# Kernel tuning notes

Hardware: AMD Instinct MI355X
Metric: run time of the kernel (lower is better)

## Reference

```python
import jax, jax.numpy as jnp
import numpy as np

HEADS = 8
DIM_HEAD = 64
SCALE = DIM_HEAD ** -0.5


def setup_inputs() -> dict:
    key = jax.random.key(0)
    ks = jax.random.split(key, 6)
    B, S, D = 4, 2048, 512
    return {
        "hidden_states": jax.random.normal(ks[0], (B, S, D), jnp.float32),
        "Wq": jax.random.normal(ks[1], (D, D), jnp.float32) * (D ** -0.5),
        "Wk": jax.random.normal(ks[2], (D, D), jnp.float32) * (D ** -0.5),
        "Wv": jax.random.normal(ks[3], (D, D), jnp.float32) * (D ** -0.5),
        "Wo": jax.random.normal(ks[4], (D, D), jnp.float32) * (D ** -0.5),
        "bo": jnp.zeros((D,), jnp.float32),
    }


def reference(hidden_states, Wq, Wk, Wv, Wo, bo):
    B, S, D = hidden_states.shape
    H, Dh = HEADS, DIM_HEAD
    # Linear projections (torch Linear: x @ W.T; weights here stored as [D, D] used directly)
    q = hidden_states @ Wq  # [B,S,D]
    k = hidden_states @ Wk
    v = hidden_states @ Wv
    # head_to_batch_dim: [B,S,D] -> [B,H,S,Dh]
    q = q.reshape(B, S, H, Dh).transpose(0, 2, 1, 3)
    k = k.reshape(B, S, H, Dh).transpose(0, 2, 1, 3)
    v = v.reshape(B, S, H, Dh).transpose(0, 2, 1, 3)
    # scaled dot-product attention, scores materialized as in baddbmm path
    scores = jnp.einsum("bhqd,bhkd->bhqk", q, k) * SCALE  # [B,H,S,S]
    probs = jax.nn.softmax(scores, axis=-1)
    out = jnp.einsum("bhqk,bhkd->bhqd", probs, v)  # [B,H,S,Dh]
    # batch_to_head_dim: [B,H,S,Dh] -> [B,S,D]
    out = out.transpose(0, 2, 1, 3).reshape(B, S, D)
    # output projection (Dropout with p=0 is identity)
    return out @ Wo + bo
```

## Files before the change

kernel.cpp:

```cpp
#include <hip/hip_runtime.h>
#include <cstdint>
#include <cstddef>


typedef __bf16 bf16;
typedef __bf16 bf16x4_t __attribute__((ext_vector_type(4)));
typedef __bf16 bf16x8_t __attribute__((ext_vector_type(8)));
typedef float  floatx4  __attribute__((ext_vector_type(4)));
typedef short  shortx4  __attribute__((ext_vector_type(4)));

#define NB   4
#define SEQ  2048
#define DM   512
#define NH   8
#define DH   64
#define MTOT (NB * SEQ)


__device__ __forceinline__ void gload16(const void* g, void* l) {
    __builtin_amdgcn_global_load_lds((const __attribute__((address_space(1))) unsigned int*)g,
                                     (__attribute__((address_space(3))) unsigned int*)l,
                                     16, 0, 0);
}

__device__ __forceinline__ shortx4 pack4(floatx4 v) {
    union { bf16x4_t h; shortx4 s; } u;
    u.h = (bf16x4_t){ (bf16)v[0], (bf16)v[1], (bf16)v[2], (bf16)v[3] };
    return u.s;
}

__global__ __launch_bounds__(256) void cvt_x(const float* __restrict__ x, bf16* __restrict__ xb) {
    int i = (blockIdx.x * 256 + threadIdx.x) * 4;
    float4 v = *(const float4*)(x + i);
    bf16x4_t o = { (bf16)v.x, (bf16)v.y, (bf16)v.z, (bf16)v.w };
    *(bf16x4_t*)(xb + i) = o;
}

__global__ __launch_bounds__(256) void prep_w(const float* __restrict__ Wq, const float* __restrict__ Wk,
                                              const float* __restrict__ Wv, const float* __restrict__ Wo,
                                              bf16* __restrict__ Wqkvt, bf16* __restrict__ Wot) {
    __shared__ float T[64][65];
    const int tid = threadIdx.x;
    const int m = blockIdx.z;
    const int k0 = blockIdx.x * 64, n0 = blockIdx.y * 64;
    const float* W = (m == 0) ? Wq : (m == 1) ? Wk : (m == 2) ? Wv : Wo;
    const float scale = (m == 0) ? 0.18033688011112042f : 1.0f;
#pragma unroll
    for (int p = 0; p < 4; p++) {
        int row = p * 16 + (tid >> 4), col = (tid & 15) * 4;
        float4 v = *(const float4*)(W + (size_t)(k0 + row) * DM + n0 + col);
        T[row][col + 0] = v.x * scale; T[row][col + 1] = v.y * scale;
        T[row][col + 2] = v.z * scale; T[row][col + 3] = v.w * scale;
    }
    __syncthreads();
#pragma unroll
    for (int p = 0; p < 4; p++) {
        int nr = p * 16 + (tid >> 4), kc = (tid & 15) * 4;
        bf16x4_t o = { (bf16)T[kc][nr], (bf16)T[kc + 1][nr], (bf16)T[kc + 2][nr], (bf16)T[kc + 3][nr] };
        bf16* dst = (m < 3) ? (Wqkvt + ((size_t)(m * DM + n0 + nr)) * DM + k0 + kc)
                            : (Wot + (size_t)(n0 + nr) * DM + k0 + kc);
        *(bf16x4_t*)dst = o;
    }
}

__global__ __launch_bounds__(256) void gemm_bt(
        const bf16* __restrict__ A, const bf16* __restrict__ Bt, int Kd, int mode,
        bf16* __restrict__ Qh, bf16* __restrict__ Kh, bf16* __restrict__ Vt,
        const float* __restrict__ bo, float* __restrict__ out) {
    __shared__ __attribute__((aligned(16))) bf16 As[128 * 64];
    __shared__ __attribute__((aligned(16))) bf16 Bs[128 * 64];
    const int tid = threadIdx.x;
    const int wave = tid >> 6, lane = tid & 63;
    const int l15 = lane & 15, quad = lane >> 4, h7 = l15 & 7;
    const int m0 = blockIdx.x * 128, n0 = blockIdx.y * 128;
    const int mw = (wave >> 1) * 64, nw = (wave & 1) * 64;
    const int srow = lane >> 3, sc = (lane & 7) ^ srow;

    floatx4 zero = {0.f, 0.f, 0.f, 0.f};
    floatx4 acc[4][4];
#pragma unroll
    for (int i = 0; i < 4; i++)
#pragma unroll
        for (int j = 0; j < 4; j++) acc[i][j] = zero;

    for (int k0 = 0; k0 < Kd; k0 += 64) {
#pragma unroll
        for (int t = 0; t < 4; t++) {
            int row = wave * 32 + t * 8 + srow;
            gload16(A  + (size_t)(m0 + row) * Kd + k0 + sc * 8, As + (wave * 32 + t * 8) * 64);
            gload16(Bt + (size_t)(n0 + row) * Kd + k0 + sc * 8, Bs + (wave * 32 + t * 8) * 64);
        }
        __syncthreads();
#pragma unroll
        for (int ks = 0; ks < 2; ks++) {
            bf16x8_t af[4], bfr[4];
#pragma unroll
            for (int i = 0; i < 4; i++)
                af[i] = *(const bf16x8_t*)(As + (mw + i * 16 + l15) * 64 + (((ks * 4 + quad) ^ h7) * 8));
#pragma unroll
            for (int j = 0; j < 4; j++)
                bfr[j] = *(const bf16x8_t*)(Bs + (nw + j * 16 + l15) * 64 + (((ks * 4 + quad) ^ h7) * 8));
#pragma unroll
            for (int i = 0; i < 4; i++)
#pragma unroll
                for (int j = 0; j < 4; j++)
                    acc[i][j] = __builtin_amdgcn_mfma_f32_16x16x32_bf16(af[i], bfr[j], acc[i][j], 0, 0, 0);
        }
        __syncthreads();
    }

#pragma unroll
    for (int i = 0; i < 4; i++) {
#pragma unroll
        for (int j = 0; j < 4; j++) {
#pragma unroll
            for (int r = 0; r < 4; r++) {
                int m = m0 + mw + i * 16 + quad * 4 + r;
                int n = n0 + nw + j * 16 + l15;
                float v = acc[i][j][r];
                if (mode == 0) {
                    int b = m >> 11, s = m & (SEQ - 1);
                    int sect = n >> 9, h = (n >> 6) & 7, d = n & 63;
                    size_t bhh = (size_t)(b * NH + h);
                    if (sect == 0)      Qh[(bhh * SEQ + s) * DH + d] = (bf16)v;
                    else if (sect == 1) Kh[(bhh * SEQ + s) * DH + d] = (bf16)v;
                    else                Vt[(bhh * DH + d) * SEQ + s] = (bf16)v;
                } else {
                    out[(size_t)m * DM + n] = v + bo[n];
                }
            }
        }
    }
}

__global__ __launch_bounds__(256) void flash_attn(
        const bf16* __restrict__ Q, const bf16* __restrict__ Kh,
        const bf16* __restrict__ Vt, bf16* __restrict__ Ob) {
    __shared__ __attribute__((aligned(16))) bf16 KV[2][2][64 * 64];
    const int tid = threadIdx.x;
    const int wave = tid >> 6, lane = tid & 63;
    const int l15 = lane & 15, quad = lane >> 4, h7 = l15 & 7;
    const int qt = blockIdx.x & 15, bh = blockIdx.x >> 4;
    const int q0 = qt * 128;
    const bf16* Kb = Kh + (size_t)bh * SEQ * DH;
    const bf16* Vb = Vt + (size_t)bh * DH * SEQ;

    bf16x8_t aq[2][2];
#pragma unroll
    for (int sub = 0; sub < 2; sub++) {
        const bf16* qr = Q + ((size_t)bh * SEQ + q0 + wave * 32 + sub * 16 + l15) * DH;
        aq[sub][0] = *(const bf16x8_t*)(qr + quad * 8);
        aq[sub][1] = *(const bf16x8_t*)(qr + 32 + quad * 8);
    }

    const int srow = lane >> 3, sc = (lane & 7) ^ srow;
    auto stage = [&](int buf, int kv0) {
#pragma unroll
        for (int t = 0; t < 2; t++) {
            int row = wave * 16 + t * 8 + srow;
            gload16(Kb + (size_t)(kv0 + row) * DH + sc * 8, &KV[buf][0][(wave * 16 + t * 8) * 64]);
            gload16(Vb + (size_t)row * SEQ + kv0 + sc * 8,  &KV[buf][1][(wave * 16 + t * 8) * 64]);
        }
    };

    floatx4 zero = {0.f, 0.f, 0.f, 0.f};
    floatx4 oacc[2][4];
    float l_run[2] = {0.f, 0.f};
#pragma unroll
    for (int sub = 0; sub < 2; sub++)
#pragma unroll
        for (int d = 0; d < 4; d++) oacc[sub][d] = zero;

    stage(0, 0);
    for (int it = 0; it < SEQ / 64; it++) {
        __syncthreads();
        if (it + 1 < SEQ / 64) stage((it + 1) & 1, (it + 1) * 64);
        const bf16* Ks = &KV[it & 1][0][0];
        const bf16* Vs = &KV[it & 1][1][0];

        floatx4 st[2][4];
#pragma unroll
        for (int ns = 0; ns < 4; ns++) {
            const bf16* kr = Ks + (ns * 16 + l15) * 64;
            bf16x8_t k0 = *(const bf16x8_t*)(kr + ((quad ^ h7) * 8));
            bf16x8_t k1 = *(const bf16x8_t*)(kr + (((4 + quad) ^ h7) * 8));
#pragma unroll
            for (int sub = 0; sub < 2; sub++) {
                floatx4 a = zero;
                a = __builtin_amdgcn_mfma_f32_16x16x32_bf16(k0, aq[sub][0], a, 0, 0, 0);
                a = __builtin_amdgcn_mfma_f32_16x16x32_bf16(k1, aq[sub][1], a, 0, 0, 0);
                st[sub][ns] = a;
            }
        }
#pragma unroll
        for (int sub = 0; sub < 2; sub++) {
            float s = 0.f;
#pragma unroll
            for (int ns = 0; ns < 4; ns++) {
#pragma unroll
                for (int r = 0; r < 4; r++) {
                    float p = __builtin_amdgcn_exp2f(st[sub][ns][r]);
                    st[sub][ns][r] = p;
                    s += p;
                }
            }
            l_run[sub] += s;
        }
#pragma unroll
        for (int c = 0; c < 4; c++) {
            shortx4 ap[2];
#pragma unroll
            for (int sub = 0; sub < 2; sub++) ap[sub] = pack4(st[sub][c]);
#pragma unroll
            for (int d = 0; d < 4; d++) {
                const bf16* vr = Vs + (d * 16 + l15) * 64;
                int cc = 2 * c + (quad >> 1);
                shortx4 bv = *(const shortx4*)(vr + ((cc ^ h7) * 8) + (quad & 1) * 4);
#pragma unroll
                for (int sub = 0; sub < 2; sub++)
                    oacc[sub][d] = __builtin_amdgcn_mfma_f32_16x16x16bf16_1k(ap[sub], bv, oacc[sub][d], 0, 0, 0);
            }
        }
    }

    float lf[2];
#pragma unroll
    for (int sub = 0; sub < 2; sub++) {
        float l = l_run[sub];
        l += __shfl_xor(l, 16, 64);
        l += __shfl_xor(l, 32, 64);
        lf[sub] = l;
    }
    const int b = bh >> 3, h = bh & 7;
#pragma unroll
    for (int sub = 0; sub < 2; sub++) {
        float linv[4];
#pragma unroll
        for (int r = 0; r < 4; r++) linv[r] = 1.0f / __shfl(lf[sub], quad * 4 + r, 64);
#pragma unroll
        for (int d = 0; d < 4; d++)
#pragma unroll
            for (int r = 0; r < 4; r++) {
                int s = q0 + wave * 32 + sub * 16 + quad * 4 + r;
                Ob[((size_t)b * SEQ + s) * DM + h * DH + d * 16 + l15] = (bf16)(oacc[sub][d][r] * linv[r]);
            }
    }
}

extern "C" void kernel_launch(void* const* d_in, const int* in_sizes, int n_in,
                              void* d_out, int out_size, void* d_ws, size_t ws_size,
                              hipStream_t stream) {
    const float* X  = (const float*)d_in[0];
    const float* Wq = (const float*)d_in[1];
    const float* Wk = (const float*)d_in[2];
    const float* Wv = (const float*)d_in[3];
    const float* Wo = (const float*)d_in[4];
    const float* bo = (const float*)d_in[5];
    float* out = (float*)d_out;

    char* ws = (char*)d_ws;
    bf16* Xb    = (bf16*)(ws + 0);
    bf16* Wqkvt = (bf16*)(ws + 8388608);
    bf16* Wot   = (bf16*)(ws + 9961472);
    bf16* Qh    = (bf16*)(ws + 10485760);
    bf16* Kh    = (bf16*)(ws + 18874368);
    bf16* Vt    = (bf16*)(ws + 27262976);
    bf16* Ob    = (bf16*)(ws + 35651584);

    cvt_x<<<MTOT * DM / 1024, 256, 0, stream>>>(X, Xb);
    prep_w<<<dim3(8, 8, 4), 256, 0, stream>>>(Wq, Wk, Wv, Wo, Wqkvt, Wot);
    gemm_bt<<<dim3(MTOT / 128, 1536 / 128), 256, 0, stream>>>(Xb, Wqkvt, DM, 0,
                                                              Qh, Kh, Vt, nullptr, nullptr);
    flash_attn<<<NB * NH * (SEQ / 128), 256, 0, stream>>>(Qh, Kh, Vt, Ob);
    gemm_bt<<<dim3(MTOT / 128, DM / 128), 256, 0, stream>>>(Ob, Wot, DM, 1,
                                                            nullptr, nullptr, nullptr, bo, out);
}
```

Measured before the change: 185.2 us.

## Split KV across wave pairs in attention and coalesce GEMM epilogues via LDS

Flash attention now gives each wave 64 query rows and half of every KV tile. It stages two KV tiles per barrier and merges the partial accumulators and row sums through shared memory at the end. The QKV projection stages its output tile in LDS so Q/K/V (including transposed V) are written with 16-byte coalesced stores instead of scattered 2-byte writes. The output projection uses smaller 64-row tiles to launch more blocks. This adds register pressure and a final LDS reduction step in attention.

```diff
diff --git a/kernel.cpp b/kernel.cpp
--- a/kernel.cpp
+++ b/kernel.cpp
@@ -8,6 +8,7 @@
 typedef __bf16 bf16x8_t __attribute__((ext_vector_type(8)));
 typedef float  floatx4  __attribute__((ext_vector_type(4)));
 typedef short  shortx4  __attribute__((ext_vector_type(4)));
+typedef uint32_t u32x4  __attribute__((ext_vector_type(4)));
 
 #define NB   4
 #define SEQ  2048
@@ -63,12 +64,11 @@
     }
 }
 
-__global__ __launch_bounds__(256) void gemm_bt(
-        const bf16* __restrict__ A, const bf16* __restrict__ Bt, int Kd, int mode,
-        bf16* __restrict__ Qh, bf16* __restrict__ Kh, bf16* __restrict__ Vt,
-        const float* __restrict__ bo, float* __restrict__ out) {
-    __shared__ __attribute__((aligned(16))) bf16 As[128 * 64];
-    __shared__ __attribute__((aligned(16))) bf16 Bs[128 * 64];
+__global__ __launch_bounds__(256) void gemm_qkv(
+        const bf16* __restrict__ A, const bf16* __restrict__ Bt,
+        bf16* __restrict__ Qh, bf16* __restrict__ Kh, bf16* __restrict__ Vt) {
+    __shared__ __attribute__((aligned(16))) bf16 Sm[2][128 * 64];
+    bf16* As = Sm[0]; bf16* Bs = Sm[1];
     const int tid = threadIdx.x;
     const int wave = tid >> 6, lane = tid & 63;
     const int l15 = lane & 15, quad = lane >> 4, h7 = l15 & 7;
@@ -83,12 +83,12 @@
 #pragma unroll
         for (int j = 0; j < 4; j++) acc[i][j] = zero;
 
-    for (int k0 = 0; k0 < Kd; k0 += 64) {
+    for (int k0 = 0; k0 < DM; k0 += 64) {
 #pragma unroll
         for (int t = 0; t < 4; t++) {
             int row = wave * 32 + t * 8 + srow;
-            gload16(A  + (size_t)(m0 + row) * Kd + k0 + sc * 8, As + (wave * 32 + t * 8) * 64);
-            gload16(Bt + (size_t)(n0 + row) * Kd + k0 + sc * 8, Bs + (wave * 32 + t * 8) * 64);
+            gload16(A  + (size_t)(m0 + row) * DM + k0 + sc * 8, As + (wave * 32 + t * 8) * 64);
+            gload16(Bt + (size_t)(n0 + row) * DM + k0 + sc * 8, Bs + (wave * 32 + t * 8) * 64);
         }
         __syncthreads();
 #pragma unroll
@@ -109,46 +109,140 @@
         __syncthreads();
     }
 
-#pragma unroll
-    for (int i = 0; i < 4; i++) {
-#pragma unroll
-        for (int j = 0; j < 4; j++) {
-#pragma unroll
-            for (int r = 0; r < 4; r++) {
-                int m = m0 + mw + i * 16 + quad * 4 + r;
-                int n = n0 + nw + j * 16 + l15;
-                float v = acc[i][j][r];
-                if (mode == 0) {
-                    int b = m >> 11, s = m & (SEQ - 1);
-                    int sect = n >> 9, h = (n >> 6) & 7, d = n & 63;
-                    size_t bhh = (size_t)(b * NH + h);
-                    if (sect == 0)      Qh[(bhh * SEQ + s) * DH + d] = (bf16)v;
-                    else if (sect == 1) Kh[(bhh * SEQ + s) * DH + d] = (bf16)v;
-                    else                Vt[(bhh * DH + d) * SEQ + s] = (bf16)v;
-                } else {
-                    out[(size_t)m * DM + n] = v + bo[n];
-                }
-            }
-        }
-    }
-}
-
-__global__ __launch_bounds__(256) void flash_attn(
-        const bf16* __restrict__ Q, const bf16* __restrict__ Kh,
-        const bf16* __restrict__ Vt, bf16* __restrict__ Ob) {
-    __shared__ __attribute__((aligned(16))) bf16 KV[2][2][64 * 64];
+    bf16* E = (bf16*)Sm;
+    const int sect = n0 >> 9;
+    const int bq = m0 >> 11;
+    if (sect < 3 && (n0 >> 9) != 2) {}
+    if (sect != 2) {
+        bf16* dstbase = (sect == 0) ? Qh : Kh;
+#pragma unroll
+        for (int p = 0; p < 2; p++) {
+            if ((wave >> 1) == p) {
+#pragma unroll
+                for (int i = 0; i < 4; i++)
+#pragma unroll
+                    for (int j = 0; j < 4; j++)
+#pragma unroll
+                        for (int r = 0; r < 4; r++)
+                            E[(i * 16 + quad * 4 + r) * 136 + nw + j * 16 + l15] = (bf16)acc[i][j][r];
+            }
+            __syncthreads();
+#pragma unroll
+            for (int pp = 0; pp < 4; pp++) {
+                int idx = pp * 256 + tid;
+                int rowl = idx >> 4, chunk = idx & 15;
+                u32x4 v = *(const u32x4*)(E + rowl * 136 + chunk * 8);
+                int mm = m0 + p * 64 + rowl;
+                int s = mm & (SEQ - 1);
+                int n = n0 + chunk * 8;
+                int h = (n >> 6) & 7, d = n & 63;
+                *(u32x4*)(dstbase + (((size_t)(bq * NH + h)) * SEQ + s) * DH + d) = v;
+            }
+            __syncthreads();
+        }
+    } else {
+#pragma unroll
+        for (int p = 0; p < 2; p++) {
+            if ((wave & 1) == p) {
+#pragma unroll
+                for (int i = 0; i < 4; i++)
+#pragma unroll
+                    for (int j = 0; j < 4; j++)
+                        *(shortx4*)(E + (j * 16 + l15) * 136 + mw + i * 16 + quad * 4) = pack4(acc[i][j]);
+            }
+            __syncthreads();
+#pragma unroll
+            for (int pp = 0; pp < 4; pp++) {
+                int idx = pp * 256 + tid;
+                int rowl = idx >> 4, chunk = idx & 15;
+                u32x4 v = *(const u32x4*)(E + rowl * 136 + chunk * 8);
+                int n = n0 + p * 64 + rowl;
+                int h = (n >> 6) & 7, d = n & 63;
+                int s = (m0 & (SEQ - 1)) + chunk * 8;
+                *(u32x4*)(Vt + (((size_t)(bq * NH + h)) * DH + d) * SEQ + s) = v;
+            }
+            __syncthreads();
+        }
+    }
+}
+
+__global__ __launch_bounds__(256) void gemm_out(
+        const bf16* __restrict__ A, const bf16* __restrict__ Bt,
+        const float* __restrict__ bo, float* __restrict__ out) {
+    __shared__ __attribute__((aligned(16))) bf16 As[64 * 64];
+    __shared__ __attribute__((aligned(16))) bf16 Bs[128 * 64];
     const int tid = threadIdx.x;
     const int wave = tid >> 6, lane = tid & 63;
     const int l15 = lane & 15, quad = lane >> 4, h7 = l15 & 7;
+    const int m0 = blockIdx.x * 64, n0 = blockIdx.y * 128;
+    const int nw = wave * 32;
+    const int srow = lane >> 3, sc = (lane & 7) ^ srow;
+
+    floatx4 zero = {0.f, 0.f, 0.f, 0.f};
+    floatx4 acc[4][2];
+#pragma unroll
+    for (int i = 0; i < 4; i++)
+#pragma unroll
+        for (int j = 0; j < 2; j++) acc[i][j] = zero;
+
+    for (int k0 = 0; k0 < DM; k0 += 64) {
+#pragma unroll
+        for (int t = 0; t < 2; t++) {
+            int row = wave * 16 + t * 8 + srow;
+            gload16(A + (size_t)(m0 + row) * DM + k0 + sc * 8, As + (wave * 16 + t * 8) * 64);
+        }
+#pragma unroll
+        for (int t = 0; t < 4; t++) {
+            int row = wave * 32 + t * 8 + srow;
+            gload16(Bt + (size_t)(n0 + row) * DM + k0 + sc * 8, Bs + (wave * 32 + t * 8) * 64);
+        }
+        __syncthreads();
+#pragma unroll
+        for (int ks = 0; ks < 2; ks++) {
+            bf16x8_t af[4], bfr[2];
+#pragma unroll
+            for (int i = 0; i < 4; i++)
+                af[i] = *(const bf16x8_t*)(As + (i * 16 + l15) * 64 + (((ks * 4 + quad) ^ h7) * 8));
+#pragma unroll
+            for (int j = 0; j < 2; j++)
+                bfr[j] = *(const bf16x8_t*)(Bs + (nw + j * 16 + l15) * 64 + (((ks * 4 + quad) ^ h7) * 8));
+#pragma unroll
+            for (int i = 0; i < 4; i++)
+#pragma unroll
+                for (int j = 0; j < 2; j++)
+                    acc[i][j] = __builtin_amdgcn_mfma_f32_16x16x32_bf16(af[i], bfr[j], acc[i][j], 0, 0, 0);
+        }
+        __syncthreads();
+    }
+#pragma unroll
+    for (int i = 0; i < 4; i++)
+#pragma unroll
+        for (int j = 0; j < 2; j++)
+#pragma unroll
+            for (int r = 0; r < 4; r++) {
+                int m = m0 + i * 16 + quad * 4 + r;
+                int n = n0 + nw + j * 16 + l15;
+                out[(size_t)m * DM + n] = acc[i][j][r] + bo[n];
+            }
+}
+
+__global__ __launch_bounds__(256, 2) void flash_attn(
+        const bf16* __restrict__ Q, const bf16* __restrict__ Kh,
+        const bf16* __restrict__ Vt, bf16* __restrict__ Ob) {
+    __shared__ __attribute__((aligned(16))) bf16 SMEM[4 * 8192];
+    const int tid = threadIdx.x;
+    const int wave = tid >> 6, lane = tid & 63;
+    const int l15 = lane & 15, quad = lane >> 4, h7 = l15 & 7;
+    const int qh = wave >> 1, kvh = wave & 1;
     const int qt = blockIdx.x & 15, bh = blockIdx.x >> 4;
     const int q0 = qt * 128;
     const bf16* Kb = Kh + (size_t)bh * SEQ * DH;
     const bf16* Vb = Vt + (size_t)bh * DH * SEQ;
 
-    bf16x8_t aq[2][2];
-#pragma unroll
-    for (int sub = 0; sub < 2; sub++) {
-        const bf16* qr = Q + ((size_t)bh * SEQ + q0 + wave * 32 + sub * 16 + l15) * DH;
+    bf16x8_t aq[4][2];
+#pragma unroll
+    for (int sub = 0; sub < 4; sub++) {
+        const bf16* qr = Q + ((size_t)bh * SEQ + q0 + qh * 64 + sub * 16 + l15) * DH;
         aq[sub][0] = *(const bf16x8_t*)(qr + quad * 8);
         aq[sub][1] = *(const bf16x8_t*)(qr + 32 + quad * 8);
     }
@@ -157,93 +251,128 @@
     auto stage = [&](int buf, int kv0) {
 #pragma unroll
         for (int t = 0; t < 2; t++) {
-            int row = wave * 16 + t * 8 + srow;
-            gload16(Kb + (size_t)(kv0 + row) * DH + sc * 8, &KV[buf][0][(wave * 16 + t * 8) * 64]);
-            gload16(Vb + (size_t)row * SEQ + kv0 + sc * 8,  &KV[buf][1][(wave * 16 + t * 8) * 64]);
+            int rb = wave * 16 + t * 8;
+            gload16(Kb + (size_t)(kv0 + rb + srow) * DH + sc * 8, SMEM + buf * 8192 + rb * 64);
+            gload16(Vb + (size_t)(rb + srow) * SEQ + kv0 + sc * 8, SMEM + buf * 8192 + 4096 + rb * 64);
         }
     };
 
     floatx4 zero = {0.f, 0.f, 0.f, 0.f};
-    floatx4 oacc[2][4];
-    float l_run[2] = {0.f, 0.f};
-#pragma unroll
-    for (int sub = 0; sub < 2; sub++)
+    floatx4 oacc[4][4];
+    float l_run[4] = {0.f, 0.f, 0.f, 0.f};
+#pragma unroll
+    for (int sub = 0; sub < 4; sub++)
 #pragma unroll
         for (int d = 0; d < 4; d++) oacc[sub][d] = zero;
 
     stage(0, 0);
-    for (int it = 0; it < SEQ / 64; it++) {
+    stage(1, 64);
+    for (int seg = 0; seg < 16; seg++) {
         __syncthreads();
-        if (it + 1 < SEQ / 64) stage((it + 1) & 1, (it + 1) * 64);
-        const bf16* Ks = &KV[it & 1][0][0];
-        const bf16* Vs = &KV[it & 1][1][0];
-
-        floatx4 st[2][4];
-#pragma unroll
-        for (int ns = 0; ns < 4; ns++) {
-            const bf16* kr = Ks + (ns * 16 + l15) * 64;
-            bf16x8_t k0 = *(const bf16x8_t*)(kr + ((quad ^ h7) * 8));
-            bf16x8_t k1 = *(const bf16x8_t*)(kr + (((4 + quad) ^ h7) * 8));
-#pragma unroll
-            for (int sub = 0; sub < 2; sub++) {
-                floatx4 a = zero;
-                a = __builtin_amdgcn_mfma_f32_16x16x32_bf16(k0, aq[sub][0], a, 0, 0, 0);
-                a = __builtin_amdgcn_mfma_f32_16x16x32_bf16(k1, aq[sub][1], a, 0, 0, 0);
-                st[sub][ns] = a;
-            }
-        }
-#pragma unroll
-        for (int sub = 0; sub < 2; sub++) {
-            float s = 0.f;
-#pragma unroll
-            for (int ns = 0; ns < 4; ns++) {
-#pragma unroll
-                for (int r = 0; r < 4; r++) {
-                    float p = __builtin_amdgcn_exp2f(st[sub][ns][r]);
-                    st[sub][ns][r] = p;
-                    s += p;
+        if (seg < 15) {
+            stage((2 * seg + 2) & 3, (2 * seg + 2) * 64);
+            stage((2 * seg + 3) & 3, (2 * seg + 3) * 64);
+        }
+#pragma unroll
+        for (int half = 0; half < 2; half++) {
+            const bf16* Ks = SMEM + ((2 * seg + half) & 3) * 8192;
+            const bf16* Vs = Ks + 4096;
+            floatx4 st[4][2];
+#pragma unroll
+            for (int nsl = 0; nsl < 2; nsl++) {
+                int row = (kvh * 2 + nsl) * 16 + l15;
+                const bf16* kr = Ks + row * 64;
+                bf16x8_t k0 = *(const bf16x8_t*)(kr + ((quad ^ h7) * 8));
+                bf16x8_t k1 = *(const bf16x8_t*)(kr + (((4 + quad) ^ h7) * 8));
+#pragma unroll
+                for (int sub = 0; sub < 4; sub++) {
+                    floatx4 a = zero;
+                    a = __builtin_amdgcn_mfma_f32_16x16x32_bf16(k0, aq[sub][0], a, 0, 0, 0);
+                    a = __builtin_amdgcn_mfma_f32_16x16x32_bf16(k1, aq[sub][1], a, 0, 0, 0);
+                    st[sub][nsl] = a;
                 }
             }
-            l_run[sub] += s;
-        }
-#pragma unroll
-        for (int c = 0; c < 4; c++) {
-            shortx4 ap[2];
-#pragma unroll
-            for (int sub = 0; sub < 2; sub++) ap[sub] = pack4(st[sub][c]);
-#pragma unroll
-            for (int d = 0; d < 4; d++) {
-                const bf16* vr = Vs + (d * 16 + l15) * 64;
+#pragma unroll
+            for (int sub = 0; sub < 4; sub++) {
+                float s = 0.f;
+#pragma unroll
+                for (int nsl = 0; nsl < 2; nsl++)
+#pragma unroll
+                    for (int r = 0; r < 4; r++) {
+                        float p = __builtin_amdgcn_exp2f(st[sub][nsl][r]);
+                        st[sub][nsl][r] = p;
+                        s += p;
+                    }
+                l_run[sub] += s;
+            }
+#pragma unroll
+            for (int cl = 0; cl < 2; cl++) {
+                int c = kvh * 2 + cl;
+                shortx4 ap[4];
+#pragma unroll
+                for (int sub = 0; sub < 4; sub++) ap[sub] = pack4(st[sub][cl]);
                 int cc = 2 * c + (quad >> 1);
-                shortx4 bv = *(const shortx4*)(vr + ((cc ^ h7) * 8) + (quad & 1) * 4);
-#pragma unroll
-                for (int sub = 0; sub < 2; sub++)
-                    oacc[sub][d] = __builtin_amdgcn_mfma_f32_16x16x16bf16_1k(ap[sub], bv, oacc[sub][d], 0, 0, 0);
-            }
-        }
-    }
-
-    float lf[2];
-#pragma unroll
-    for (int sub = 0; sub < 2; sub++) {
+#pragma unroll
+                for (int d = 0; d < 4; d++) {
+                    const bf16* vr = Vs + (d * 16 + l15) * 64;
+                    shortx4 bv = *(const shortx4*)(vr + ((cc ^ h7) * 8) + (quad & 1) * 4);
+#pragma unroll
+                    for (int sub = 0; sub < 4; sub++)
+                        oacc[sub][d] = __builtin_amdgcn_mfma_f32_16x16x16bf16_1k(ap[sub], bv, oacc[sub][d], 0, 0, 0);
+                }
+            }
+        }
+    }
+
+    float lf[4];
+#pragma unroll
+    for (int sub = 0; sub < 4; sub++) {
         float l = l_run[sub];
         l += __shfl_xor(l, 16, 64);
         l += __shfl_xor(l, 32, 64);
         lf[sub] = l;
     }
-    const int b = bh >> 3, h = bh & 7;
-#pragma unroll
-    for (int sub = 0; sub < 2; sub++) {
-        float linv[4];
-#pragma unroll
-        for (int r = 0; r < 4; r++) linv[r] = 1.0f / __shfl(lf[sub], quad * 4 + r, 64);
-#pragma unroll
-        for (int d = 0; d < 4; d++)
-#pragma unroll
-            for (int r = 0; r < 4; r++) {
-                int s = q0 + wave * 32 + sub * 16 + quad * 4 + r;
-                Ob[((size_t)b * SEQ + s) * DM + h * DH + d * 16 + l15] = (bf16)(oacc[sub][d][r] * linv[r]);
-            }
+    __syncthreads();
+    float* blob = (float*)SMEM + qh * (68 * 64);
+    if (kvh == 1) {
+#pragma unroll
+        for (int sub = 0; sub < 4; sub++)
+#pragma unroll
+            for (int d = 0; d < 4; d++)
+#pragma unroll
+                for (int r = 0; r < 4; r++)
+                    blob[((sub * 4 + d) * 4 + r) * 64 + lane] = oacc[sub][d][r];
+#pragma unroll
+        for (int sub = 0; sub < 4; sub++)
+            blob[(64 + sub) * 64 + lane] = lf[sub];
+    }
+    __syncthreads();
+    if (kvh == 0) {
+#pragma unroll
+        for (int sub = 0; sub < 4; sub++)
+#pragma unroll
+            for (int d = 0; d < 4; d++)
+#pragma unroll
+                for (int r = 0; r < 4; r++)
+                    oacc[sub][d][r] += blob[((sub * 4 + d) * 4 + r) * 64 + lane];
+#pragma unroll
+        for (int sub = 0; sub < 4; sub++)
+            lf[sub] += blob[(64 + sub) * 64 + lane];
+
+        const int b = bh >> 3, h = bh & 7;
+#pragma unroll
+        for (int sub = 0; sub < 4; sub++) {
+            float linv[4];
+#pragma unroll
+            for (int r = 0; r < 4; r++) linv[r] = 1.0f / __shfl(lf[sub], quad * 4 + r, 64);
+#pragma unroll
+            for (int d = 0; d < 4; d++)
+#pragma unroll
+                for (int r = 0; r < 4; r++) {
+                    int s = q0 + qh * 64 + sub * 16 + quad * 4 + r;
+                    Ob[((size_t)b * SEQ + s) * DM + h * DH + d * 16 + l15] = (bf16)(oacc[sub][d][r] * linv[r]);
+                }
+        }
     }
 }
 
@@ -269,9 +398,7 @@
 
     cvt_x<<<MTOT * DM / 1024, 256, 0, stream>>>(X, Xb);
     prep_w<<<dim3(8, 8, 4), 256, 0, stream>>>(Wq, Wk, Wv, Wo, Wqkvt, Wot);
-    gemm_bt<<<dim3(MTOT / 128, 1536 / 128), 256, 0, stream>>>(Xb, Wqkvt, DM, 0,
-                                                              Qh, Kh, Vt, nullptr, nullptr);
+    gemm_qkv<<<dim3(MTOT / 128, 1536 / 128), 256, 0, stream>>>(Xb, Wqkvt, Qh, Kh, Vt);
     flash_attn<<<NB * NH * (SEQ / 128), 256, 0, stream>>>(Qh, Kh, Vt, Ob);
-    gemm_bt<<<dim3(MTOT / 128, DM / 128), 256, 0, stream>>>(Ob, Wot, DM, 1,
-                                                            nullptr, nullptr, nullptr, bo, out);
-}
+    gemm_out<<<dim3(MTOT / 64, DM / 128), 256, 0, stream>>>(Ob, Wot, bo, out);
+}
```

Result: faster. 160.7 us (-13.2%).
